# Performance work log

Measured on AMD Instinct MI355X. Metric: run time of the kernel, lower is better.

Reference implementation:

```python
import jax, jax.numpy as jnp
import numpy as np

S, B, V, E, H, C = 512, 64, 50000, 300, 256, 5


def setup_inputs() -> dict:
    key = jax.random.key(0)
    ks = jax.random.split(key, 8)
    return {
        "inputs": jax.random.randint(ks[0], (S, B), 0, V, dtype=jnp.int64),
        "emb": jax.random.normal(ks[1], (V, E), dtype=jnp.float32),
        # small weight scale to keep tanh out of saturation (matches typical init scale)
        "W_ih": jax.random.normal(ks[2], (H, E), dtype=jnp.float32) * 0.05,
        "W_hh": jax.random.normal(ks[3], (H, H), dtype=jnp.float32) * 0.05,
        "b_ih": jax.random.normal(ks[4], (H,), dtype=jnp.float32) * 0.05,
        "b_hh": jax.random.normal(ks[5], (H,), dtype=jnp.float32) * 0.05,
        "W_out": jax.random.normal(ks[6], (C, H), dtype=jnp.float32) * 0.05,
        "b_out": jax.random.normal(ks[7], (C,), dtype=jnp.float32) * 0.05,
    }


def reference(inputs, emb, W_ih, W_hh, b_ih, b_hh, W_out, b_out):
    # embedding lookup: (S, B, E)
    x = emb[inputs]
    # precompute input-to-hidden projection for all timesteps: (S, B, H)
    xW = jnp.einsum("sbe,he->sbh", x, W_ih) + b_ih

    def step(h, xw_t):
        h_new = jnp.tanh(xw_t + h @ W_hh.T + b_hh)
        return h_new, h_new

    h0 = jnp.zeros((inputs.shape[1], W_hh.shape[0]), dtype=x.dtype)
    _, rnn_out = jax.lax.scan(step, h0, xW)  # (S, B, H)

    logits = jnp.einsum("sbh,ch->sbc", rnn_out, W_out) + b_out  # (S, B, C)
    summed = logits.sum(axis=0)  # (B, C)
    return jax.nn.log_softmax(summed, axis=1)
```

## Files before the change

kernel.cpp:

```cpp
#include <hip/hip_runtime.h>
#include <stdint.h>

#define S_ 512
#define B_ 64
#define V_ 50000
#define E_ 300
#define H_ 256
#define C_ 5

typedef _Float16 h8_t __attribute__((ext_vector_type(8)));
typedef float f32x4 __attribute__((ext_vector_type(4)));

__device__ __forceinline__ float fast_tanh(float x) {
    float e = __builtin_amdgcn_exp2f(x * 2.88539008177793f);
    return fmaf(-2.0f, __builtin_amdgcn_rcpf(e + 1.0f), 1.0f);
}

__global__ void wb_prep_kernel(const float* __restrict__ W_ih,
                               uint4* __restrict__ WB) {
    int g = blockIdx.x * 256 + threadIdx.x;
    if (g >= 16 * 10 * 64) return;
    int l = g & 63;
    int ks = (g >> 6) % 10;
    int nt = g / 640;
    int h = nt * 16 + (l & 15);
    int e0 = ks * 32 + (l >> 4) * 8;
    h8_t v;
#pragma unroll
    for (int j = 0; j < 8; ++j) {
        int e = e0 + j;
        v[j] = (e < E_) ? (_Float16)W_ih[(size_t)h * E_ + e] : (_Float16)0.0f;
    }
    WB[g] = __builtin_bit_cast(uint4, v);
}

__global__ __launch_bounds__(512, 2) void xw_kernel(
    const int* __restrict__ idx, const float* __restrict__ emb,
    const uint4* __restrict__ WB, const float* __restrict__ b_ih,
    const float* __restrict__ b_hh, float* __restrict__ xw) {
    __shared__ uint4 Afrag[4 * 10 * 64];
    const int tid = threadIdx.x;
    const int w = tid >> 6;
    const int l = tid & 63;
    const int n = l & 15;
    const int hi = l >> 4;
    const int base = blockIdx.x * 64;

    for (int cc = tid; cc < 64 * 40; cc += 512) {
        int m = cc / 40;
        int c = cc - m * 40;
        int ks = c >> 2;
        int hic = c & 3;
        const float* src = emb + (size_t)idx[base + m] * E_ + 8 * c;
        h8_t v;
        if (c < 37) {
            float4 f0 = *(const float4*)src;
            float4 f1 = *(const float4*)(src + 4);
            v[0] = (_Float16)f0.x; v[1] = (_Float16)f0.y;
            v[2] = (_Float16)f0.z; v[3] = (_Float16)f0.w;
            v[4] = (_Float16)f1.x; v[5] = (_Float16)f1.y;
            v[6] = (_Float16)f1.z; v[7] = (_Float16)f1.w;
        } else if (c == 37) {
            float4 f0 = *(const float4*)src;
            v[0] = (_Float16)f0.x; v[1] = (_Float16)f0.y;
            v[2] = (_Float16)f0.z; v[3] = (_Float16)f0.w;
            v[4] = (_Float16)0.0f; v[5] = (_Float16)0.0f;
            v[6] = (_Float16)0.0f; v[7] = (_Float16)0.0f;
        } else {
            v = (h8_t)(_Float16)0.0f;
        }
        int fl = (hic << 4) | (m & 15);
        int mt = m >> 4;
        Afrag[(mt * 10 + ks) * 64 + fl] = __builtin_bit_cast(uint4, v);
    }
    __syncthreads();

    float bias0 = b_ih[w * 32 + n] + b_hh[w * 32 + n];
    float bias1 = b_ih[w * 32 + 16 + n] + b_hh[w * 32 + 16 + n];
    f32x4 c[4][2];
#pragma unroll
    for (int mt = 0; mt < 4; ++mt) {
        c[mt][0] = (f32x4)bias0;
        c[mt][1] = (f32x4)bias1;
    }

    const uint4* wb0 = WB + ((2 * w) * 10) * 64 + l;
    const uint4* wb1 = WB + ((2 * w + 1) * 10) * 64 + l;
#pragma unroll
    for (int ks = 0; ks < 10; ++ks) {
        h8_t b0 = __builtin_bit_cast(h8_t, wb0[ks * 64]);
        h8_t b1 = __builtin_bit_cast(h8_t, wb1[ks * 64]);
#pragma unroll
        for (int mt = 0; mt < 4; ++mt) {
            h8_t a = __builtin_bit_cast(h8_t, Afrag[(mt * 10 + ks) * 64 + l]);
            c[mt][0] = __builtin_amdgcn_mfma_f32_16x16x32_f16(a, b0, c[mt][0],
                                                              0, 0, 0);
            c[mt][1] = __builtin_amdgcn_mfma_f32_16x16x32_f16(a, b1, c[mt][1],
                                                              0, 0, 0);
        }
    }

#pragma unroll
    for (int mt = 0; mt < 4; ++mt)
#pragma unroll
        for (int q = 0; q < 2; ++q) {
            float* op =
                xw + (size_t)(base + mt * 16 + hi * 4) * H_ + w * 32 + q * 16 + n;
#pragma unroll
            for (int r = 0; r < 4; ++r) op[(size_t)r * H_] = c[mt][q][r];
        }
}

__global__ __launch_bounds__(512, 2) void rnn_kernel(
    const float* __restrict__ xw, const float* __restrict__ W_hh,
    float* __restrict__ hsum_out) {
    const int tid = threadIdx.x;
    const int w = tid >> 6;
    const int l = tid & 63;
    const int n = l & 15;
    const int hi = l >> 4;
    const int bbase = blockIdx.x * 16;
    const int rowbase = w * 32;

    __shared__ __attribute__((aligned(16))) unsigned char Hl[2][8192];
    char* lds = (char*)Hl;

    h8_t a[2][8];
#pragma unroll
    for (int mt = 0; mt < 2; ++mt) {
        const float* wr = W_hh + (size_t)(rowbase + mt * 16 + n) * H_;
#pragma unroll
        for (int ks = 0; ks < 8; ++ks) {
            const float* wp = wr + ks * 32 + hi * 8;
            float4 f0 = *(const float4*)wp;
            float4 f1 = *(const float4*)(wp + 4);
            h8_t v;
            v[0] = (_Float16)f0.x; v[1] = (_Float16)f0.y;
            v[2] = (_Float16)f0.z; v[3] = (_Float16)f0.w;
            v[4] = (_Float16)f1.x; v[5] = (_Float16)f1.y;
            v[6] = (_Float16)f1.z; v[7] = (_Float16)f1.w;
            a[mt][ks] = v;
        }
    }

    int wboff[2];
#pragma unroll
    for (int mt = 0; mt < 2; ++mt) {
        int k0 = rowbase + mt * 16 + hi * 4;
        wboff[mt] = ((k0 >> 5) << 10) + (((k0 >> 3) & 3) << 8) + (n << 4) +
                    ((k0 & 7) << 1);
    }

    for (int t = tid; t < 2048; t += 512) ((unsigned int*)Hl)[t] = 0u;

    f32x4 hs[2];
    hs[0] = (f32x4)0.0f;
    hs[1] = (f32x4)0.0f;

    const float* xwl = xw + (size_t)(bbase + n) * H_ + rowbase + hi * 4;
    f32x4 cv[4][2];
    cv[0][0] = *(const f32x4*)(xwl);
    cv[0][1] = *(const f32x4*)(xwl + 16);
    cv[1][0] = *(const f32x4*)(xwl + 16384);
    cv[1][1] = *(const f32x4*)(xwl + 16384 + 16);
    __syncthreads();

#define STEP(CUR, I, SBASE)                                                    \
    {                                                                          \
                     \
        int sp = (SBASE) + 2;                                                  \
        if (sp > S_ - 1) sp = S_ - 1;                                          \
        cv[(I + 2) & 3][0] = *(const f32x4*)(xwl + (size_t)sp * 16384);        \
        cv[(I + 2) & 3][1] = *(const f32x4*)(xwl + (size_t)sp * 16384 + 16);   \
        h8_t bf[8];                                                            \
        _Pragma("unroll") for (int ks = 0; ks < 8; ++ks)                       \
            bf[ks] = *(const h8_t*)(lds + (CUR)*8192 + ks * 1024 + l * 16);    \
        _Pragma("unroll") for (int ks = 0; ks < 8; ++ks) {                     \
            cv[I][0] = __builtin_amdgcn_mfma_f32_16x16x32_f16(                 \
                a[0][ks], bf[ks], cv[I][0], 0, 0, 0);                          \
            cv[I][1] = __builtin_amdgcn_mfma_f32_16x16x32_f16(                 \
                a[1][ks], bf[ks], cv[I][1], 0, 0, 0);                          \
        }                                                                      \
        _Pragma("unroll") for (int mt = 0; mt < 2; ++mt) {                     \
            float h0 = fast_tanh(cv[I][mt][0]);                                \
            float h1 = fast_tanh(cv[I][mt][1]);                                \
            float h2 = fast_tanh(cv[I][mt][2]);                                \
            float h3 = fast_tanh(cv[I][mt][3]);                                \
            hs[mt][0] += h0; hs[mt][1] += h1;                                  \
            hs[mt][2] += h2; hs[mt][3] += h3;                                  \
            uint2 pk;                                                          \
            pk.x = __builtin_bit_cast(unsigned int,                            \
                                      __builtin_amdgcn_cvt_pkrtz(h0, h1));     \
            pk.y = __builtin_bit_cast(unsigned int,                            \
                                      __builtin_amdgcn_cvt_pkrtz(h2, h3));     \
            *(uint2*)(lds + ((CUR) ^ 1) * 8192 + wboff[mt]) = pk;              \
        }                                                                      \
        asm volatile("s_waitcnt lgkmcnt(0)" ::: "memory");                     \
        __builtin_amdgcn_s_barrier();                                          \
    }

    for (int s = 0; s < S_; s += 4) {
        STEP(0, 0, s)
        STEP(1, 1, s + 1)
        STEP(0, 2, s + 2)
        STEP(1, 3, s + 3)
    }
#undef STEP

#pragma unroll
    for (int mt = 0; mt < 2; ++mt) {
        float4 o;
        o.x = hs[mt][0]; o.y = hs[mt][1]; o.z = hs[mt][2]; o.w = hs[mt][3];
        *(float4*)(hsum_out + (size_t)(bbase + n) * H_ + rowbase + mt * 16 +
                   hi * 4) = o;
    }
}

__global__ void out_kernel(const float* __restrict__ hsum,
                           const float* __restrict__ W_out,
                           const float* __restrict__ b_out,
                           float* __restrict__ out) {
    int b = threadIdx.x;
    if (b >= B_) return;
    float logits[C_];
#pragma unroll
    for (int c = 0; c < C_; ++c) {
        float acc = 0.0f;
        for (int k = 0; k < H_; ++k)
            acc = fmaf(hsum[b * H_ + k], W_out[c * H_ + k], acc);
        logits[c] = acc + (float)S_ * b_out[c];
    }
    float m = logits[0];
#pragma unroll
    for (int c = 1; c < C_; ++c) m = fmaxf(m, logits[c]);
    float sum = 0.0f;
#pragma unroll
    for (int c = 0; c < C_; ++c) sum += expf(logits[c] - m);
    float lse = logf(sum);
#pragma unroll
    for (int c = 0; c < C_; ++c) out[b * C_ + c] = logits[c] - m - lse;
}

extern "C" void kernel_launch(void* const* d_in, const int* in_sizes, int n_in,
                              void* d_out, int out_size, void* d_ws,
                              size_t ws_size, hipStream_t stream) {
    const int* idx = (const int*)d_in[0];
    const float* emb = (const float*)d_in[1];
    const float* W_ih = (const float*)d_in[2];
    const float* W_hh = (const float*)d_in[3];
    const float* b_ih = (const float*)d_in[4];
    const float* b_hh = (const float*)d_in[5];
    const float* W_out = (const float*)d_in[6];
    const float* b_out = (const float*)d_in[7];
    float* out = (float*)d_out;

    float* ws = (float*)d_ws;
    uint4* WB = (uint4*)ws;
    float* xw = ws + 40960;
    float* hsum = xw + (size_t)S_ * B_ * H_;

    hipLaunchKernelGGL(wb_prep_kernel, dim3(40), dim3(256), 0, stream, W_ih,
                       WB);
    hipLaunchKernelGGL(xw_kernel, dim3((S_ * B_) / 64), dim3(512), 0, stream,
                       idx, emb, WB, b_ih, b_hh, xw);
    hipLaunchKernelGGL(rnn_kernel, dim3(4), dim3(512), 0, stream, xw, W_hh,
                       hsum);
    hipLaunchKernelGGL(out_kernel, dim3(1), dim3(64), 0, stream, hsum, W_out,
                       b_out, out);
}
```

Baseline: 324.7 us.

## Fuse xW projection and RNN recurrence into one kernel with counter-based handoff

Merges the input-projection kernel and the recurrent kernel into a single launch. Blocks 0-3 run the serial RNN while the remaining 512 blocks compute xW tiles. Each producer block bumps a per-group atomic counter (8 timesteps per group), and the RNN blocks spin on that counter before prefetching each new group. The aim is to overlap the sequential recurrence with the projection GEMM and drop one kernel boundary. This adds a memset and relies on the low-index RNN blocks being co-resident with producers, with a spin-wait and sleep on the critical path.

```diff
diff --git a/kernel.cpp b/kernel.cpp
--- a/kernel.cpp
+++ b/kernel.cpp
@@ -14,6 +14,14 @@
 __device__ __forceinline__ float fast_tanh(float x) {
     float e = __builtin_amdgcn_exp2f(x * 2.88539008177793f);
     return fmaf(-2.0f, __builtin_amdgcn_rcpf(e + 1.0f), 1.0f);
+}
+
+__device__ __forceinline__ void wait_group(unsigned* gcnt, int grp) {
+    while (__hip_atomic_load(&gcnt[grp], __ATOMIC_RELAXED,
+                             __HIP_MEMORY_SCOPE_AGENT) != 8u) {
+        __builtin_amdgcn_s_sleep(16);
+    }
+    __builtin_amdgcn_fence(__ATOMIC_ACQUIRE, "agent");
 }
 
 __global__ void wb_prep_kernel(const float* __restrict__ W_ih,
@@ -34,87 +42,97 @@
     WB[g] = __builtin_bit_cast(uint4, v);
 }
 
-__global__ __launch_bounds__(512, 2) void xw_kernel(
+__global__ __launch_bounds__(512, 2) void fused_kernel(
     const int* __restrict__ idx, const float* __restrict__ emb,
     const uint4* __restrict__ WB, const float* __restrict__ b_ih,
-    const float* __restrict__ b_hh, float* __restrict__ xw) {
-    __shared__ uint4 Afrag[4 * 10 * 64];
+    const float* __restrict__ b_hh, float* __restrict__ xw,
+    const float* __restrict__ W_hh, float* __restrict__ hsum_out,
+    unsigned* __restrict__ gcnt) {
+    __shared__ __attribute__((aligned(16))) unsigned char smem[40960];
     const int tid = threadIdx.x;
-    const int w = tid >> 6;
-    const int l = tid & 63;
-    const int n = l & 15;
-    const int hi = l >> 4;
-    const int base = blockIdx.x * 64;
-
-    for (int cc = tid; cc < 64 * 40; cc += 512) {
-        int m = cc / 40;
-        int c = cc - m * 40;
-        int ks = c >> 2;
-        int hic = c & 3;
-        const float* src = emb + (size_t)idx[base + m] * E_ + 8 * c;
-        h8_t v;
-        if (c < 37) {
-            float4 f0 = *(const float4*)src;
-            float4 f1 = *(const float4*)(src + 4);
-            v[0] = (_Float16)f0.x; v[1] = (_Float16)f0.y;
-            v[2] = (_Float16)f0.z; v[3] = (_Float16)f0.w;
-            v[4] = (_Float16)f1.x; v[5] = (_Float16)f1.y;
-            v[6] = (_Float16)f1.z; v[7] = (_Float16)f1.w;
-        } else if (c == 37) {
-            float4 f0 = *(const float4*)src;
-            v[0] = (_Float16)f0.x; v[1] = (_Float16)f0.y;
-            v[2] = (_Float16)f0.z; v[3] = (_Float16)f0.w;
-            v[4] = (_Float16)0.0f; v[5] = (_Float16)0.0f;
-            v[6] = (_Float16)0.0f; v[7] = (_Float16)0.0f;
-        } else {
-            v = (h8_t)(_Float16)0.0f;
-        }
-        int fl = (hic << 4) | (m & 15);
-        int mt = m >> 4;
-        Afrag[(mt * 10 + ks) * 64 + fl] = __builtin_bit_cast(uint4, v);
-    }
-    __syncthreads();
-
-    float bias0 = b_ih[w * 32 + n] + b_hh[w * 32 + n];
-    float bias1 = b_ih[w * 32 + 16 + n] + b_hh[w * 32 + 16 + n];
-    f32x4 c[4][2];
-#pragma unroll
-    for (int mt = 0; mt < 4; ++mt) {
-        c[mt][0] = (f32x4)bias0;
-        c[mt][1] = (f32x4)bias1;
-    }
-
-    const uint4* wb0 = WB + ((2 * w) * 10) * 64 + l;
-    const uint4* wb1 = WB + ((2 * w + 1) * 10) * 64 + l;
-#pragma unroll
-    for (int ks = 0; ks < 10; ++ks) {
-        h8_t b0 = __builtin_bit_cast(h8_t, wb0[ks * 64]);
-        h8_t b1 = __builtin_bit_cast(h8_t, wb1[ks * 64]);
+
+    if (blockIdx.x >= 4) {
+        const int g = blockIdx.x - 4;
+        uint4* Afrag = (uint4*)smem;
+        const int w = tid >> 6;
+        const int l = tid & 63;
+        const int n = l & 15;
+        const int hi = l >> 4;
+        const int base = g * 64;
+
+        for (int cc = tid; cc < 64 * 40; cc += 512) {
+            int m = cc / 40;
+            int c = cc - m * 40;
+            int ks = c >> 2;
+            int hic = c & 3;
+            const float* src = emb + (size_t)idx[base + m] * E_ + 8 * c;
+            h8_t v;
+            if (c < 37) {
+                float4 f0 = *(const float4*)src;
+                float4 f1 = *(const float4*)(src + 4);
+                v[0] = (_Float16)f0.x; v[1] = (_Float16)f0.y;
+                v[2] = (_Float16)f0.z; v[3] = (_Float16)f0.w;
+                v[4] = (_Float16)f1.x; v[5] = (_Float16)f1.y;
+                v[6] = (_Float16)f1.z; v[7] = (_Float16)f1.w;
+            } else if (c == 37) {
+                float4 f0 = *(const float4*)src;
+                v[0] = (_Float16)f0.x; v[1] = (_Float16)f0.y;
+                v[2] = (_Float16)f0.z; v[3] = (_Float16)f0.w;
+                v[4] = (_Float16)0.0f; v[5] = (_Float16)0.0f;
+                v[6] = (_Float16)0.0f; v[7] = (_Float16)0.0f;
+            } else {
+                v = (h8_t)(_Float16)0.0f;
+            }
+            int fl = (hic << 4) | (m & 15);
+            int mt = m >> 4;
+            Afrag[(mt * 10 + ks) * 64 + fl] = __builtin_bit_cast(uint4, v);
+        }
+        __syncthreads();
+
+        float bias0 = b_ih[w * 32 + n] + b_hh[w * 32 + n];
+        float bias1 = b_ih[w * 32 + 16 + n] + b_hh[w * 32 + 16 + n];
+        f32x4 c[4][2];
 #pragma unroll
         for (int mt = 0; mt < 4; ++mt) {
-            h8_t a = __builtin_bit_cast(h8_t, Afrag[(mt * 10 + ks) * 64 + l]);
-            c[mt][0] = __builtin_amdgcn_mfma_f32_16x16x32_f16(a, b0, c[mt][0],
-                                                              0, 0, 0);
-            c[mt][1] = __builtin_amdgcn_mfma_f32_16x16x32_f16(a, b1, c[mt][1],
-                                                              0, 0, 0);
-        }
-    }
-
-#pragma unroll
-    for (int mt = 0; mt < 4; ++mt)
-#pragma unroll
-        for (int q = 0; q < 2; ++q) {
-            float* op =
-                xw + (size_t)(base + mt * 16 + hi * 4) * H_ + w * 32 + q * 16 + n;
-#pragma unroll
-            for (int r = 0; r < 4; ++r) op[(size_t)r * H_] = c[mt][q][r];
-        }
-}
-
-__global__ __launch_bounds__(512, 2) void rnn_kernel(
-    const float* __restrict__ xw, const float* __restrict__ W_hh,
-    float* __restrict__ hsum_out) {
-    const int tid = threadIdx.x;
+            c[mt][0] = (f32x4)bias0;
+            c[mt][1] = (f32x4)bias1;
+        }
+
+        const uint4* wb0 = WB + ((2 * w) * 10) * 64 + l;
+        const uint4* wb1 = WB + ((2 * w + 1) * 10) * 64 + l;
+#pragma unroll
+        for (int ks = 0; ks < 10; ++ks) {
+            h8_t b0 = __builtin_bit_cast(h8_t, wb0[ks * 64]);
+            h8_t b1 = __builtin_bit_cast(h8_t, wb1[ks * 64]);
+#pragma unroll
+            for (int mt = 0; mt < 4; ++mt) {
+                h8_t a =
+                    __builtin_bit_cast(h8_t, Afrag[(mt * 10 + ks) * 64 + l]);
+                c[mt][0] = __builtin_amdgcn_mfma_f32_16x16x32_f16(a, b0,
+                                                                  c[mt][0], 0, 0, 0);
+                c[mt][1] = __builtin_amdgcn_mfma_f32_16x16x32_f16(a, b1,
+                                                                  c[mt][1], 0, 0, 0);
+            }
+        }
+
+#pragma unroll
+        for (int mt = 0; mt < 4; ++mt)
+#pragma unroll
+            for (int q = 0; q < 2; ++q) {
+                float* op = xw + (size_t)(base + mt * 16 + hi * 4) * H_ +
+                            w * 32 + q * 16 + n;
+#pragma unroll
+                for (int r = 0; r < 4; ++r) op[(size_t)r * H_] = c[mt][q][r];
+            }
+
+        __syncthreads();
+        if (tid == 0) {
+            __threadfence();
+            atomicAdd(&gcnt[g >> 3], 1u);
+        }
+        return;
+    }
+
     const int w = tid >> 6;
     const int l = tid & 63;
     const int n = l & 15;
@@ -122,8 +140,7 @@
     const int bbase = blockIdx.x * 16;
     const int rowbase = w * 32;
 
-    __shared__ __attribute__((aligned(16))) unsigned char Hl[2][8192];
-    char* lds = (char*)Hl;
+    char* lds = (char*)smem;
 
     h8_t a[2][8];
 #pragma unroll
@@ -151,11 +168,13 @@
                     ((k0 & 7) << 1);
     }
 
-    for (int t = tid; t < 2048; t += 512) ((unsigned int*)Hl)[t] = 0u;
+    for (int t = tid; t < 2048; t += 512) ((unsigned int*)lds)[t] = 0u;
 
     f32x4 hs[2];
     hs[0] = (f32x4)0.0f;
     hs[1] = (f32x4)0.0f;
+
+    wait_group(gcnt, 0);
 
     const float* xwl = xw + (size_t)(bbase + n) * H_ + rowbase + hi * 4;
     f32x4 cv[4][2];
@@ -167,8 +186,8 @@
 
 #define STEP(CUR, I, SBASE)                                                    \
     {                                                                          \
-                     \
         int sp = (SBASE) + 2;                                                  \
+        if ((sp & 7) == 0 && sp < S_) wait_group(gcnt, sp >> 3);               \
         if (sp > S_ - 1) sp = S_ - 1;                                          \
         cv[(I + 2) & 3][0] = *(const f32x4*)(xwl + (size_t)sp * 16384);        \
         cv[(I + 2) & 3][1] = *(const f32x4*)(xwl + (size_t)sp * 16384 + 16);   \
@@ -258,13 +277,13 @@
     uint4* WB = (uint4*)ws;
     float* xw = ws + 40960;
     float* hsum = xw + (size_t)S_ * B_ * H_;
-
+    unsigned* gcnt = (unsigned*)(hsum + B_ * H_);
+
+    hipMemsetAsync(gcnt, 0, 64 * sizeof(unsigned), stream);
     hipLaunchKernelGGL(wb_prep_kernel, dim3(40), dim3(256), 0, stream, W_ih,
                        WB);
-    hipLaunchKernelGGL(xw_kernel, dim3((S_ * B_) / 64), dim3(512), 0, stream,
-                       idx, emb, WB, b_ih, b_hh, xw);
-    hipLaunchKernelGGL(rnn_kernel, dim3(4), dim3(512), 0, stream, xw, W_hh,
-                       hsum);
+    hipLaunchKernelGGL(fused_kernel, dim3(516), dim3(512), 0, stream, idx, emb,
+                       WB, b_ih, b_hh, xw, W_hh, hsum, gcnt);
     hipLaunchKernelGGL(out_kernel, dim3(1), dim3(64), 0, stream, hsum, W_out,
                        b_out, out);
 }
```

Result: slower. 361.7 us (+11.4%).

## Split RNN batch across eight blocks with duplicated MFMA columns

Applied to the files above, without the earlier changes.

The recurrent kernel now handles 8 batch columns per block instead of 16 and launches 8 blocks. Each 16-wide MFMA B operand is filled by two copies of the 8 columns, and each lane selects one of the two M-tile results to apply tanh and write back. The aim is to halve the per-step tanh and LDS work per wave and spread the serial recurrence over more CUs. In exchange, half of the MFMA throughput is wasted on duplicate columns, and the per-step barrier latency is unchanged.

```diff
diff --git a/kernel.cpp b/kernel.cpp
--- a/kernel.cpp
+++ b/kernel.cpp
@@ -119,10 +119,12 @@
     const int l = tid & 63;
     const int n = l & 15;
     const int hi = l >> 4;
-    const int bbase = blockIdx.x * 16;
+    const int col = n & 7;
+    const int sel = n >> 3;
+    const int bbase = blockIdx.x * 8;
     const int rowbase = w * 32;
 
-    __shared__ __attribute__((aligned(16))) unsigned char Hl[2][8192];
+    __shared__ __attribute__((aligned(16))) unsigned char Hl[2][4096];
     char* lds = (char*)Hl;
 
     h8_t a[2][8];
@@ -143,21 +145,15 @@
         }
     }
 
-    int wboff[2];
-#pragma unroll
-    for (int mt = 0; mt < 2; ++mt) {
-        int k0 = rowbase + mt * 16 + hi * 4;
-        wboff[mt] = ((k0 >> 5) << 10) + (((k0 >> 3) & 3) << 8) + (n << 4) +
-                    ((k0 & 7) << 1);
-    }
-
-    for (int t = tid; t < 2048; t += 512) ((unsigned int*)Hl)[t] = 0u;
-
-    f32x4 hs[2];
-    hs[0] = (f32x4)0.0f;
-    hs[1] = (f32x4)0.0f;
-
-    const float* xwl = xw + (size_t)(bbase + n) * H_ + rowbase + hi * 4;
+    const int wboff =
+        (w * 4 + sel * 2 + (hi >> 1)) * 128 + col * 16 + (hi & 1) * 8;
+    const int rdbase = hi * 128 + col * 16;
+
+    for (int t = tid; t < 1024; t += 512) ((unsigned int*)Hl)[t] = 0u;
+
+    f32x4 hs = (f32x4)0.0f;
+
+    const float* xwl = xw + (size_t)(bbase + col) * H_ + rowbase + hi * 4;
     f32x4 cv[4][2];
     cv[0][0] = *(const f32x4*)(xwl);
     cv[0][1] = *(const f32x4*)(xwl + 16);
@@ -167,33 +163,32 @@
 
 #define STEP(CUR, I, SBASE)                                                    \
     {                                                                          \
-                     \
         int sp = (SBASE) + 2;                                                  \
         if (sp > S_ - 1) sp = S_ - 1;                                          \
         cv[(I + 2) & 3][0] = *(const f32x4*)(xwl + (size_t)sp * 16384);        \
         cv[(I + 2) & 3][1] = *(const f32x4*)(xwl + (size_t)sp * 16384 + 16);   \
         h8_t bf[8];                                                            \
         _Pragma("unroll") for (int ks = 0; ks < 8; ++ks)                       \
-            bf[ks] = *(const h8_t*)(lds + (CUR)*8192 + ks * 1024 + l * 16);    \
+            bf[ks] = *(const h8_t*)(lds + (CUR)*4096 + rdbase + ks * 512);     \
         _Pragma("unroll") for (int ks = 0; ks < 8; ++ks) {                     \
             cv[I][0] = __builtin_amdgcn_mfma_f32_16x16x32_f16(                 \
                 a[0][ks], bf[ks], cv[I][0], 0, 0, 0);                          \
             cv[I][1] = __builtin_amdgcn_mfma_f32_16x16x32_f16(                 \
                 a[1][ks], bf[ks], cv[I][1], 0, 0, 0);                          \
         }                                                                      \
-        _Pragma("unroll") for (int mt = 0; mt < 2; ++mt) {                     \
-            float h0 = fast_tanh(cv[I][mt][0]);                                \
-            float h1 = fast_tanh(cv[I][mt][1]);                                \
-            float h2 = fast_tanh(cv[I][mt][2]);                                \
-            float h3 = fast_tanh(cv[I][mt][3]);                                \
-            hs[mt][0] += h0; hs[mt][1] += h1;                                  \
-            hs[mt][2] += h2; hs[mt][3] += h3;                                  \
+        {                                                                      \
+            f32x4 sv = (sel == 0) ? cv[I][0] : cv[I][1];                       \
+            float h0 = fast_tanh(sv[0]);                                       \
+            float h1 = fast_tanh(sv[1]);                                       \
+            float h2 = fast_tanh(sv[2]);                                       \
+            float h3 = fast_tanh(sv[3]);                                       \
+            hs[0] += h0; hs[1] += h1; hs[2] += h2; hs[3] += h3;                \
             uint2 pk;                                                          \
             pk.x = __builtin_bit_cast(unsigned int,                            \
                                       __builtin_amdgcn_cvt_pkrtz(h0, h1));     \
             pk.y = __builtin_bit_cast(unsigned int,                            \
                                       __builtin_amdgcn_cvt_pkrtz(h2, h3));     \
-            *(uint2*)(lds + ((CUR) ^ 1) * 8192 + wboff[mt]) = pk;              \
+            *(uint2*)(lds + ((CUR) ^ 1) * 4096 + wboff) = pk;                  \
         }                                                                      \
         asm volatile("s_waitcnt lgkmcnt(0)" ::: "memory");                     \
         __builtin_amdgcn_s_barrier();                                          \
@@ -207,11 +202,10 @@
     }
 #undef STEP
 
-#pragma unroll
-    for (int mt = 0; mt < 2; ++mt) {
+    {
         float4 o;
-        o.x = hs[mt][0]; o.y = hs[mt][1]; o.z = hs[mt][2]; o.w = hs[mt][3];
-        *(float4*)(hsum_out + (size_t)(bbase + n) * H_ + rowbase + mt * 16 +
+        o.x = hs[0]; o.y = hs[1]; o.z = hs[2]; o.w = hs[3];
+        *(float4*)(hsum_out + (size_t)(bbase + col) * H_ + rowbase + sel * 16 +
                    hi * 4) = o;
     }
 }
@@ -263,7 +257,7 @@
                        WB);
     hipLaunchKernelGGL(xw_kernel, dim3((S_ * B_) / 64), dim3(512), 0, stream,
                        idx, emb, WB, b_ih, b_hh, xw);
-    hipLaunchKernelGGL(rnn_kernel, dim3(4), dim3(512), 0, stream, xw, W_hh,
+    hipLaunchKernelGGL(rnn_kernel, dim3(8), dim3(512), 0, stream, xw, W_hh,
                        hsum);
     hipLaunchKernelGGL(out_kernel, dim3(1), dim3(64), 0, stream, hsum, W_out,
                        b_out, out);
```

Result: faster. 281.4 us (-13.3%).
